# Performance work log

Measured on AMD Instinct MI355X. Metric: run time of the kernel, lower is better.

## Reference

```python
import jax, jax.numpy as jnp
import numpy as np

NUM_HEADS = 16
D_MODEL = 1024
D_K = D_MODEL // NUM_HEADS


def setup_inputs() -> dict:
    key = jax.random.key(0)
    ks = jax.random.split(key, 12)
    B, S = 2, 2048
    scale = 1.0 / np.sqrt(D_MODEL)
    inp = {
        "query": jax.random.normal(ks[0], (B, S, D_MODEL), jnp.float32),
        "key": jax.random.normal(ks[1], (B, S, D_MODEL), jnp.float32),
        "value": jax.random.normal(ks[2], (B, S, D_MODEL), jnp.float32),
        "mask": jnp.ones((B, S, S), jnp.int32),
        "Wq": jax.random.normal(ks[3], (D_MODEL, D_MODEL), jnp.float32) * scale,
        "bq": jax.random.normal(ks[4], (D_MODEL,), jnp.float32) * scale,
        "Wk": jax.random.normal(ks[5], (D_MODEL, D_MODEL), jnp.float32) * scale,
        "bk": jax.random.normal(ks[6], (D_MODEL,), jnp.float32) * scale,
        "Wv": jax.random.normal(ks[7], (D_MODEL, D_MODEL), jnp.float32) * scale,
        "bv": jax.random.normal(ks[8], (D_MODEL,), jnp.float32) * scale,
        "Wo": jax.random.normal(ks[9], (D_MODEL, D_MODEL), jnp.float32) * scale,
        "bo": jax.random.normal(ks[10], (D_MODEL,), jnp.float32) * scale,
    }
    return inp


def _split_heads(x):
    B, S, _ = x.shape
    return x.reshape(B, S, NUM_HEADS, D_K).transpose(0, 2, 1, 3)  # [B,H,S,d_k]


def reference(query, key, value, mask, Wq, bq, Wk, bk, Wv, bv, Wo, bo):
    # torch Linear: y = x @ W.T + b
    q = _split_heads(query @ Wq.T + bq)
    k = _split_heads(key @ Wk.T + bk)
    v = _split_heads(value @ Wv.T + bv)
    scores = jnp.einsum("bhqd,bhkd->bhqk", q, k) / np.sqrt(D_K)
    scores = jnp.where(mask[:, None, :, :] == 0, jnp.float32(-1e9), scores)
    p_attn = jax.nn.softmax(scores, axis=-1)
    attn = jnp.einsum("bhqk,bhkd->bhqd", p_attn, v)  # [B,H,S,d_k]
    B, _, S, _ = attn.shape
    x = attn.transpose(0, 2, 1, 3).reshape(B, S, D_MODEL)
    return x @ Wo.T + bo
```

## Files before the change

### kernel.cpp

```cpp
#include <hip/hip_runtime.h>
#include <hip/hip_bf16.h>
#include <cstdint>

#define DEVINL static __device__ __forceinline__

typedef __attribute__((ext_vector_type(4))) float floatx4;
typedef __attribute__((ext_vector_type(8))) short bf16x8;

DEVINL unsigned short f2bf(float f) {
    union { float f; uint32_t u; } v; v.f = f;
    return (unsigned short)((v.u + 0x7FFFu + ((v.u >> 16) & 1u)) >> 16);
}

DEVINL uint32_t pk2bf(float x, float y) {
    __hip_bfloat162 h = __float22bfloat162_rn(float2{x, y});
    union { __hip_bfloat162 h; uint32_t u; } v; v.h = h;
    return v.u;
}

DEVINL floatx4 mfma16(bf16x8 a, bf16x8 b, floatx4 c) {
    return __builtin_amdgcn_mfma_f32_16x16x32_bf16(a, b, c, 0, 0, 0);
}

#define GLDS16(g, l)                                                            \
    __builtin_amdgcn_global_load_lds(                                           \
        (const __attribute__((address_space(1))) void*)(g),                     \
        (__attribute__((address_space(3))) void*)(l), 16, 0, 0)

constexpr int B_ = 2, S_ = 2048, D_ = 1024, H_ = 16, DK_ = 64;
constexpr int BSROWS = B_ * S_;
constexpr int NQB = S_ / 128;
constexpr int NKT = S_ / 64;

constexpr float QSCALE = 0.18033688011112042f;

__device__ int g_flags[B_ * NQB * NKT];

__global__ __launch_bounds__(256)
void prep(const float* __restrict__ q, const float* __restrict__ k,
          const float* __restrict__ v,
          const float* __restrict__ Wq, const float* __restrict__ Wk,
          const float* __restrict__ Wv, const float* __restrict__ Wo,
          unsigned short* __restrict__ qb, unsigned short* __restrict__ kb,
          unsigned short* __restrict__ vb,
          unsigned short* __restrict__ wqb, unsigned short* __restrict__ wkb,
          unsigned short* __restrict__ wvb, unsigned short* __restrict__ wob,
          const int* __restrict__ mask)
{
    __shared__ int f;
    int bid = blockIdx.x;
    if (bid < 8192) {
        const float* src; unsigned short* dst; int rb;
        if      (bid < 2048) { src = q;  dst = qb;  rb = bid; }
        else if (bid < 4096) { src = k;  dst = kb;  rb = bid - 2048; }
        else if (bid < 6144) { src = v;  dst = vb;  rb = bid - 4096; }
        else if (bid < 6656) { src = Wq; dst = wqb; rb = bid - 6144; }
        else if (bid < 7168) { src = Wk; dst = wkb; rb = bid - 6656; }
        else if (bid < 7680) { src = Wv; dst = wvb; rb = bid - 7168; }
        else                 { src = Wo; dst = wob; rb = bid - 7680; }
        size_t e = ((size_t)rb * 256 + threadIdx.x) * 8;
        float4 v0 = *(const float4*)(src + e);
        float4 v1 = *(const float4*)(src + e + 4);
        uint4 o;
        o.x = pk2bf(v0.x, v0.y); o.y = pk2bf(v0.z, v0.w);
        o.z = pk2bf(v1.x, v1.y); o.w = pk2bf(v1.z, v1.w);
        *(uint4*)(dst + e) = o;
    } else {
        int mb = bid - 8192;
        int kt = mb & 31, qq = (mb >> 5) & 15, b = mb >> 9;
        const int* base = mask + (size_t)(b * S_ + qq * 128) * S_ + kt * 64;
        int ok = 1;
        #pragma unroll
        for (int i = 0; i < 8; ++i) {
            int u = threadIdx.x + 256 * i;
            int row = u >> 4, c = u & 15;
            int4 m = *(const int4*)(base + (size_t)row * S_ + c * 4);
            if ((m.x == 0) | (m.y == 0) | (m.z == 0) | (m.w == 0)) ok = 0;
        }
        if (threadIdx.x == 0) f = 1;
        __syncthreads();
        if (!ok) f = 0;
        __syncthreads();
        if (threadIdx.x == 0) g_flags[mb] = f;
    }
}

__global__ __launch_bounds__(256)
void gemm_qkv(const unsigned short* __restrict__ qb, const unsigned short* __restrict__ kb,
              const unsigned short* __restrict__ vb,
              const unsigned short* __restrict__ wqb, const unsigned short* __restrict__ wkb,
              const unsigned short* __restrict__ wvb,
              const float* __restrict__ bq, const float* __restrict__ bk,
              const float* __restrict__ bv,
              unsigned short* __restrict__ Qp, unsigned short* __restrict__ KpF,
              unsigned short* __restrict__ VpF)
{
    constexpr int K = D_, N = D_;
    __shared__ unsigned short As[2][128 * 64];
    __shared__ unsigned short Bs[2][128 * 64];

    const int bid = blockIdx.x;
    const int xcd = bid & 7, sl = bid >> 3;
    const int z = sl >> 5, rr = sl & 31;
    const int nb = rr >> 2, mloc = rr & 3;
    const int m0 = (mloc * 8 + xcd) * 128, n0 = nb * 128;

    const unsigned short* A = z == 0 ? qb  : z == 1 ? kb  : vb;
    const unsigned short* W = z == 0 ? wqb : z == 1 ? wkb : wvb;
    const float* bias       = z == 0 ? bq  : z == 1 ? bk  : bv;

    const int tid  = threadIdx.x;
    const int lane = tid & 63, wave = tid >> 6;
    const int lr = lane & 15, lg = lane >> 4;
    const int wm = (wave >> 1) * 64, wn = (wave & 1) * 64;

    int rowA[4], kcA[4];
    #pragma unroll
    for (int j = 0; j < 4; ++j) {
        int L = (wave * 4 + j) * 64 + lane;
        rowA[j] = L >> 3; kcA[j] = (L & 7) ^ (rowA[j] & 7);
    }

    auto dma = [&](int k0, int buf) {
        #pragma unroll
        for (int j = 0; j < 4; ++j)
            GLDS16(A + (size_t)(m0 + rowA[j]) * K + k0 + kcA[j] * 8,
                   &As[buf][(wave * 4 + j) * 512 + lane * 8]);
        #pragma unroll
        for (int j = 0; j < 4; ++j)
            GLDS16(W + (size_t)(n0 + rowA[j]) * K + k0 + kcA[j] * 8,
                   &Bs[buf][(wave * 4 + j) * 512 + lane * 8]);
    };

    floatx4 acc[4][4];
    #pragma unroll
    for (int mt = 0; mt < 4; ++mt)
        #pragma unroll
        for (int nt = 0; nt < 4; ++nt)
            acc[mt][nt] = floatx4{0.f, 0.f, 0.f, 0.f};

    dma(0, 0);
    for (int it = 0; it < K / 64; ++it) {
        __syncthreads();
        if (it + 1 < K / 64) dma((it + 1) * 64, (it + 1) & 1);
        const int buf = it & 1;

        #pragma unroll
        for (int kf = 0; kf < 2; ++kf) {
            bf16x8 af[4], bfr[4];
            #pragma unroll
            for (int mt = 0; mt < 4; ++mt) {
                int row = wm + mt * 16 + lr;
                af[mt] = *(const bf16x8*)&As[buf][row * 64 + (((kf * 4 + lg) ^ (lr & 7)) * 8)];
            }
            #pragma unroll
            for (int nt = 0; nt < 4; ++nt) {
                int row = wn + nt * 16 + lr;
                bfr[nt] = *(const bf16x8*)&Bs[buf][row * 64 + (((kf * 4 + lg) ^ (lr & 7)) * 8)];
            }
            #pragma unroll
            for (int mt = 0; mt < 4; ++mt)
                #pragma unroll
                for (int nt = 0; nt < 4; ++nt)
                    acc[mt][nt] = mfma16(af[mt], bfr[nt], acc[mt][nt]);
        }
    }

    if (z == 0) {
        #pragma unroll
        for (int nt = 0; nt < 4; ++nt) {
            int col = n0 + wn + nt * 16 + lr;
            float bv2 = bias[col];
            #pragma unroll
            for (int mt = 0; mt < 4; ++mt)
                #pragma unroll
                for (int reg = 0; reg < 4; ++reg) {
                    int row = m0 + wm + mt * 16 + lg * 4 + reg;
                    Qp[(size_t)row * N + col] = f2bf((acc[mt][nt][reg] + bv2) * QSCALE);
                }
        }
    } else if (z == 1) {
        #pragma unroll
        for (int nt = 0; nt < 4; ++nt) {
            int c = n0 + wn + nt * 16 + lr;
            int h = c >> 6, d = c & 63;
            int kfA = d >> 5, lgA = (d >> 3) & 3, j = d & 7;
            float bv2 = bias[c];
            #pragma unroll
            for (int mt = 0; mt < 4; ++mt)
                #pragma unroll
                for (int reg = 0; reg < 4; ++reg) {
                    int t = m0 + wm + mt * 16 + lg * 4 + reg;
                    int bb = t >> 11, sx = t & (S_ - 1);
                    int kt = sx >> 6, key = sx & 63;
                    int mtA = key >> 4, lrA = key & 15;
                    size_t off = (((size_t)(bb * 16 + h) * 32 + kt) * 8 + (kfA * 4 + mtA)) * 512
                               + (lrA + 16 * lgA) * 8 + j;
                    KpF[off] = f2bf(acc[mt][nt][reg] + bv2);
                }
        }
    } else {
        #pragma unroll
        for (int nt = 0; nt < 4; ++nt) {
            int c = n0 + wn + nt * 16 + lr;
            int h = c >> 6, dtA = (c >> 4) & 3;
            float bv2 = bias[c];
            #pragma unroll
            for (int mt = 0; mt < 4; ++mt) {
                int t0 = m0 + wm + mt * 16 + lg * 4;
                int bb = t0 >> 11, s0 = t0 & (S_ - 1);
                int kt = s0 >> 6, key = s0 & 63;
                int kfA = key >> 5, lgA = (key >> 3) & 3, j0 = key & 7;
                size_t off = (((size_t)(bb * 16 + h) * 32 + kt) * 8 + (dtA * 2 + kfA)) * 512
                           + (lr + 16 * lgA) * 8 + j0;
                uint2 p;
                p.x = pk2bf(acc[mt][nt][0] + bv2, acc[mt][nt][1] + bv2);
                p.y = pk2bf(acc[mt][nt][2] + bv2, acc[mt][nt][3] + bv2);
                *(uint2*)&VpF[off] = p;
            }
        }
    }
}

__global__ __launch_bounds__(256, 2)
void attn_flash(const unsigned short* __restrict__ Qp,
                const unsigned short* __restrict__ KpF,
                const unsigned short* __restrict__ VpF,
                const int* __restrict__ mask,
                unsigned short* __restrict__ Out)
{
    constexpr int LD = 72;
    __shared__ unsigned short Ps[128 * LD];

    const int tid = threadIdx.x;
    const int lane = tid & 63, wave = tid >> 6;
    const int lr = lane & 15, lg = lane >> 4;
    const int h = blockIdx.x, qb = blockIdx.y, b = blockIdx.z;
    const int q0 = qb * 128, qw = q0 + wave * 32;

    bf16x8 qf[2][2];
    #pragma unroll
    for (int qt = 0; qt < 2; ++qt)
        #pragma unroll
        for (int kf = 0; kf < 2; ++kf)
            qf[qt][kf] = *(const bf16x8*)(Qp + (size_t)(b * S_ + qw + qt * 16 + lr) * D_ +
                                          h * DK_ + kf * 32 + lg * 8);

    float l_[2] = {0.f, 0.f};
    floatx4 o_acc[2][4];
    #pragma unroll
    for (int qt = 0; qt < 2; ++qt)
        #pragma unroll
        for (int dt = 0; dt < 4; ++dt) o_acc[qt][dt] = floatx4{0.f, 0.f, 0.f, 0.f};

    const unsigned short* kbase = KpF + (size_t)(b * 16 + h) * 32 * 4096 + lane * 8;
    const unsigned short* vbase = VpF + (size_t)(b * 16 + h) * 32 * 4096 + lane * 8;
    const int fbase = (b * NQB + qb) * NKT;
    unsigned short* PsW = &Ps[(wave * 32 + lr) * LD];

    auto loadKV = [&](int kt, bf16x8 (&kfr)[8], bf16x8 (&vfr)[8]) {
        const unsigned short* kb = kbase + kt * 4096;
        const unsigned short* vb = vbase + kt * 4096;
        #pragma unroll
        for (int c = 0; c < 8; ++c) kfr[c] = *(const bf16x8*)(kb + c * 512);
        #pragma unroll
        for (int c = 0; c < 8; ++c) vfr[c] = *(const bf16x8*)(vb + c * 512);
    };

    auto process = [&](int kt, bf16x8 (&kfr)[8], bf16x8 (&vfr)[8]) {
        floatx4 sc[2][4];
        #pragma unroll
        for (int qt = 0; qt < 2; ++qt)
            #pragma unroll
            for (int mt = 0; mt < 4; ++mt) sc[qt][mt] = floatx4{0.f, 0.f, 0.f, 0.f};
        #pragma unroll
        for (int mt = 0; mt < 4; ++mt)
            #pragma unroll
            for (int kf = 0; kf < 2; ++kf)
                #pragma unroll
                for (int qt = 0; qt < 2; ++qt)
                    sc[qt][mt] = mfma16(kfr[kf * 4 + mt], qf[qt][kf], sc[qt][mt]);

        if (g_flags[fbase + kt] == 0) {
            #pragma unroll
            for (int qt = 0; qt < 2; ++qt) {
                int qq = qw + qt * 16 + lr;
                const int* mrow = mask + (size_t)(b * S_ + qq) * S_ + kt * 64;
                #pragma unroll
                for (int mt = 0; mt < 4; ++mt)
                    #pragma unroll
                    for (int reg = 0; reg < 4; ++reg)
                        if (mrow[mt * 16 + lg * 4 + reg] == 0)
                            sc[qt][mt][reg] = -1e9f;
            }
        }

        #pragma unroll
        for (int qt = 0; qt < 2; ++qt) {
            #pragma unroll
            for (int mt = 0; mt < 4; ++mt) {
                float p0 = __builtin_amdgcn_exp2f(sc[qt][mt][0]);
                float p1 = __builtin_amdgcn_exp2f(sc[qt][mt][1]);
                float p2 = __builtin_amdgcn_exp2f(sc[qt][mt][2]);
                float p3 = __builtin_amdgcn_exp2f(sc[qt][mt][3]);
                l_[qt] += (p0 + p1) + (p2 + p3);
                uint2 pk; pk.x = pk2bf(p0, p1); pk.y = pk2bf(p2, p3);
                *(uint2*)&PsW[qt * 16 * LD + mt * 16 + lg * 4] = pk;
            }
        }

        bf16x8 pb[2][2];
        #pragma unroll
        for (int qt = 0; qt < 2; ++qt)
            #pragma unroll
            for (int kf = 0; kf < 2; ++kf)
                pb[qt][kf] = *(const bf16x8*)&PsW[qt * 16 * LD + kf * 32 + lg * 8];
        #pragma unroll
        for (int dt = 0; dt < 4; ++dt)
            #pragma unroll
            for (int kf = 0; kf < 2; ++kf)
                #pragma unroll
                for (int qt = 0; qt < 2; ++qt)
                    o_acc[qt][dt] = mfma16(vfr[dt * 2 + kf], pb[qt][kf], o_acc[qt][dt]);
    };

    bf16x8 kA[8], vA[8], kB[8], vB[8];
    loadKV(0, kA, vA);
    for (int kt = 0; kt < NKT; kt += 2) {
        loadKV(kt + 1, kB, vB);
        process(kt, kA, vA);
        if (kt + 2 < NKT) loadKV(kt + 2, kA, vA);
        process(kt + 1, kB, vB);
    }

    #pragma unroll
    for (int qt = 0; qt < 2; ++qt) {
        float l = l_[qt];
        l += __shfl_xor(l, 16, 64);
        l += __shfl_xor(l, 32, 64);
        float inv = 1.f / l;
        int qq = qw + qt * 16 + lr;
        #pragma unroll
        for (int dt = 0; dt < 4; ++dt) {
            uint2 p;
            p.x = pk2bf(o_acc[qt][dt][0] * inv, o_acc[qt][dt][1] * inv);
            p.y = pk2bf(o_acc[qt][dt][2] * inv, o_acc[qt][dt][3] * inv);
            *(uint2*)&Out[(size_t)(b * S_ + qq) * D_ + h * DK_ + dt * 16 + lg * 4] = p;
        }
    }
}

__global__ __launch_bounds__(256)
void gemm_out(const unsigned short* __restrict__ Ap,
              const unsigned short* __restrict__ Wb,
              const float* __restrict__ bias, float* __restrict__ Cptr)
{
    constexpr int K = D_, N = D_;
    __shared__ unsigned short As[2][128 * 64];
    __shared__ unsigned short Wss[2][64 * 64];

    const int bid = blockIdx.x;
    const int xcd = bid & 7, sl = bid >> 3;
    const int nb = sl >> 2, mloc = sl & 3;
    const int m0 = (mloc * 8 + xcd) * 128, n0 = nb * 64;

    const int tid  = threadIdx.x;
    const int lane = tid & 63, wave = tid >> 6;
    const int lr = lane & 15, lg = lane >> 4;
    const int wm = (wave >> 1) * 64, wn = (wave & 1) * 32;

    int rowA[4], kcA[4], rowW[2], kcW[2];
    #pragma unroll
    for (int j = 0; j < 4; ++j) {
        int L = (wave * 4 + j) * 64 + lane;
        rowA[j] = L >> 3; kcA[j] = (L & 7) ^ (rowA[j] & 7);
    }
    #pragma unroll
    for (int j = 0; j < 2; ++j) {
        int L = (wave * 2 + j) * 64 + lane;
        rowW[j] = L >> 3; kcW[j] = (L & 7) ^ (rowW[j] & 7);
    }

    auto dma = [&](int k0, int buf) {
        #pragma unroll
        for (int j = 0; j < 4; ++j)
            GLDS16(Ap + (size_t)(m0 + rowA[j]) * K + k0 + kcA[j] * 8,
                   &As[buf][(wave * 4 + j) * 512 + lane * 8]);
        #pragma unroll
        for (int j = 0; j < 2; ++j)
            GLDS16(Wb + (size_t)(n0 + rowW[j]) * K + k0 + kcW[j] * 8,
                   &Wss[buf][(wave * 2 + j) * 512 + lane * 8]);
    };

    floatx4 acc[4][2];
    #pragma unroll
    for (int mt = 0; mt < 4; ++mt)
        #pragma unroll
        for (int nt = 0; nt < 2; ++nt)
            acc[mt][nt] = floatx4{0.f, 0.f, 0.f, 0.f};

    dma(0, 0);
    for (int it = 0; it < K / 64; ++it) {
        __syncthreads();
        if (it + 1 < K / 64) dma((it + 1) * 64, (it + 1) & 1);
        const int buf = it & 1;

        #pragma unroll
        for (int kf = 0; kf < 2; ++kf) {
            bf16x8 af[4], bfr[2];
            #pragma unroll
            for (int mt = 0; mt < 4; ++mt) {
                int row = wm + mt * 16 + lr;
                af[mt] = *(const bf16x8*)&As[buf][row * 64 + (((kf * 4 + lg) ^ (lr & 7)) * 8)];
            }
            #pragma unroll
            for (int nt = 0; nt < 2; ++nt) {
                int row = wn + nt * 16 + lr;
                bfr[nt] = *(const bf16x8*)&Wss[buf][row * 64 + (((kf * 4 + lg) ^ (lr & 7)) * 8)];
            }
            #pragma unroll
            for (int mt = 0; mt < 4; ++mt)
                #pragma unroll
                for (int nt = 0; nt < 2; ++nt)
                    acc[mt][nt] = mfma16(af[mt], bfr[nt], acc[mt][nt]);
        }
    }

    #pragma unroll
    for (int nt = 0; nt < 2; ++nt) {
        int col = n0 + wn + nt * 16 + lr;
        float bv2 = bias[col];
        #pragma unroll
        for (int mt = 0; mt < 4; ++mt)
            #pragma unroll
            for (int reg = 0; reg < 4; ++reg) {
                int row = m0 + wm + mt * 16 + lg * 4 + reg;
                Cptr[(size_t)row * N + col] = acc[mt][nt][reg] + bv2;
            }
    }
}

extern "C" void kernel_launch(void* const* d_in, const int* in_sizes, int n_in,
                              void* d_out, int out_size, void* d_ws, size_t ws_size,
                              hipStream_t stream)
{
    const float* query = (const float*)d_in[0];
    const float* key   = (const float*)d_in[1];
    const float* value = (const float*)d_in[2];
    const int*   mask  = (const int*)d_in[3];
    const float* Wq = (const float*)d_in[4];
    const float* bq = (const float*)d_in[5];
    const float* Wk = (const float*)d_in[6];
    const float* bk = (const float*)d_in[7];
    const float* Wv = (const float*)d_in[8];
    const float* bv = (const float*)d_in[9];
    const float* Wo = (const float*)d_in[10];
    const float* bo = (const float*)d_in[11];

    unsigned short* qb  = (unsigned short*)d_ws;
    unsigned short* kb  = qb  + (size_t)BSROWS * D_;
    unsigned short* vb  = kb  + (size_t)BSROWS * D_;
    unsigned short* wqb = vb  + (size_t)BSROWS * D_;
    unsigned short* wkb = wqb + (size_t)D_ * D_;
    unsigned short* wvb = wkb + (size_t)D_ * D_;
    unsigned short* wob = wvb + (size_t)D_ * D_;
    unsigned short* Qp  = wob + (size_t)D_ * D_;
    unsigned short* KpF = Qp  + (size_t)BSROWS * D_;
    unsigned short* VpF = KpF + (size_t)BSROWS * D_;
    unsigned short* Ap  = qb;

    dim3 blk(256);

    hipLaunchKernelGGL(prep, dim3(8192 + 1024), blk, 0, stream,
                       query, key, value, Wq, Wk, Wv, Wo,
                       qb, kb, vb, wqb, wkb, wvb, wob, mask);

    hipLaunchKernelGGL(gemm_qkv, dim3(768), blk, 0, stream,
                       qb, kb, vb, wqb, wkb, wvb, bq, bk, bv, Qp, KpF, VpF);

    dim3 gattn(H_, NQB, B_);
    hipLaunchKernelGGL(attn_flash, gattn, blk, 0, stream, Qp, KpF, VpF, mask, Ap);

    hipLaunchKernelGGL(gemm_out, dim3(512), blk, 0, stream, Ap, wob, bo, (float*)d_out);
}
```

Before: 260.8 us.

## Fuse fp32-to-bf16 conversion into GEMM loads and drop separate prep kernel

Removes the prep kernel that converted inputs and weights to bf16. The QKV and output GEMMs now load fp32 tiles into registers, convert them to bf16, and store them to LDS through a two-deep software pipeline. The mask-flag scan moves into extra blocks of the QKV GEMM launch. This saves one launch and the write-then-reread of bf16 copies, but the GEMMs read twice as many bytes per tile from global memory. Staging through registers also replaces the direct global-to-LDS loads and raises register pressure (launch_bounds 256,2).

After: 250.4 us. 4.0% less time.

```diff
diff --git a/kernel.cpp b/kernel.cpp
--- a/kernel.cpp
+++ b/kernel.cpp
@@ -36,78 +36,52 @@
 
 __device__ int g_flags[B_ * NQB * NKT];
 
-__global__ __launch_bounds__(256)
-void prep(const float* __restrict__ q, const float* __restrict__ k,
-          const float* __restrict__ v,
-          const float* __restrict__ Wq, const float* __restrict__ Wk,
-          const float* __restrict__ Wv, const float* __restrict__ Wo,
-          unsigned short* __restrict__ qb, unsigned short* __restrict__ kb,
-          unsigned short* __restrict__ vb,
-          unsigned short* __restrict__ wqb, unsigned short* __restrict__ wkb,
-          unsigned short* __restrict__ wvb, unsigned short* __restrict__ wob,
-          const int* __restrict__ mask)
-{
-    __shared__ int f;
-    int bid = blockIdx.x;
-    if (bid < 8192) {
-        const float* src; unsigned short* dst; int rb;
-        if      (bid < 2048) { src = q;  dst = qb;  rb = bid; }
-        else if (bid < 4096) { src = k;  dst = kb;  rb = bid - 2048; }
-        else if (bid < 6144) { src = v;  dst = vb;  rb = bid - 4096; }
-        else if (bid < 6656) { src = Wq; dst = wqb; rb = bid - 6144; }
-        else if (bid < 7168) { src = Wk; dst = wkb; rb = bid - 6656; }
-        else if (bid < 7680) { src = Wv; dst = wvb; rb = bid - 7168; }
-        else                 { src = Wo; dst = wob; rb = bid - 7680; }
-        size_t e = ((size_t)rb * 256 + threadIdx.x) * 8;
-        float4 v0 = *(const float4*)(src + e);
-        float4 v1 = *(const float4*)(src + e + 4);
-        uint4 o;
-        o.x = pk2bf(v0.x, v0.y); o.y = pk2bf(v0.z, v0.w);
-        o.z = pk2bf(v1.x, v1.y); o.w = pk2bf(v1.z, v1.w);
-        *(uint4*)(dst + e) = o;
-    } else {
-        int mb = bid - 8192;
-        int kt = mb & 31, qq = (mb >> 5) & 15, b = mb >> 9;
-        const int* base = mask + (size_t)(b * S_ + qq * 128) * S_ + kt * 64;
-        int ok = 1;
-        #pragma unroll
-        for (int i = 0; i < 8; ++i) {
-            int u = threadIdx.x + 256 * i;
-            int row = u >> 4, c = u & 15;
-            int4 m = *(const int4*)(base + (size_t)row * S_ + c * 4);
-            if ((m.x == 0) | (m.y == 0) | (m.z == 0) | (m.w == 0)) ok = 0;
-        }
-        if (threadIdx.x == 0) f = 1;
-        __syncthreads();
-        if (!ok) f = 0;
-        __syncthreads();
-        if (threadIdx.x == 0) g_flags[mb] = f;
-    }
-}
-
-__global__ __launch_bounds__(256)
-void gemm_qkv(const unsigned short* __restrict__ qb, const unsigned short* __restrict__ kb,
-              const unsigned short* __restrict__ vb,
-              const unsigned short* __restrict__ wqb, const unsigned short* __restrict__ wkb,
-              const unsigned short* __restrict__ wvb,
+__global__ __launch_bounds__(256, 2)
+void gemm_qkv(const float* __restrict__ q, const float* __restrict__ k,
+              const float* __restrict__ v,
+              const float* __restrict__ Wq, const float* __restrict__ Wk,
+              const float* __restrict__ Wv,
               const float* __restrict__ bq, const float* __restrict__ bk,
               const float* __restrict__ bv,
+              const int* __restrict__ mask,
               unsigned short* __restrict__ Qp, unsigned short* __restrict__ KpF,
               unsigned short* __restrict__ VpF)
 {
     constexpr int K = D_, N = D_;
     __shared__ unsigned short As[2][128 * 64];
     __shared__ unsigned short Bs[2][128 * 64];
+    __shared__ int fflag;
 
     const int bid = blockIdx.x;
+
+    if (bid >= 768) {
+        int mb = bid - 768;
+        int kt = mb & 31, qq = (mb >> 5) & 15, b = mb >> 9;
+        const int* base = mask + (size_t)(b * S_ + qq * 128) * S_ + kt * 64;
+        int ok = 1;
+        #pragma unroll
+        for (int i = 0; i < 8; ++i) {
+            int u = threadIdx.x + 256 * i;
+            int row = u >> 4, c = u & 15;
+            int4 m = *(const int4*)(base + (size_t)row * S_ + c * 4);
+            if ((m.x == 0) | (m.y == 0) | (m.z == 0) | (m.w == 0)) ok = 0;
+        }
+        if (threadIdx.x == 0) fflag = 1;
+        __syncthreads();
+        if (!ok) fflag = 0;
+        __syncthreads();
+        if (threadIdx.x == 0) g_flags[mb] = fflag;
+        return;
+    }
+
     const int xcd = bid & 7, sl = bid >> 3;
     const int z = sl >> 5, rr = sl & 31;
     const int nb = rr >> 2, mloc = rr & 3;
     const int m0 = (mloc * 8 + xcd) * 128, n0 = nb * 128;
 
-    const unsigned short* A = z == 0 ? qb  : z == 1 ? kb  : vb;
-    const unsigned short* W = z == 0 ? wqb : z == 1 ? wkb : wvb;
-    const float* bias       = z == 0 ? bq  : z == 1 ? bk  : bv;
+    const float* A    = z == 0 ? q  : z == 1 ? k  : v;
+    const float* W    = z == 0 ? Wq : z == 1 ? Wk : Wv;
+    const float* bias = z == 0 ? bq : z == 1 ? bk : bv;
 
     const int tid  = threadIdx.x;
     const int lane = tid & 63, wave = tid >> 6;
@@ -121,15 +95,30 @@
         rowA[j] = L >> 3; kcA[j] = (L & 7) ^ (rowA[j] & 7);
     }
 
-    auto dma = [&](int k0, int buf) {
-        #pragma unroll
-        for (int j = 0; j < 4; ++j)
-            GLDS16(A + (size_t)(m0 + rowA[j]) * K + k0 + kcA[j] * 8,
-                   &As[buf][(wave * 4 + j) * 512 + lane * 8]);
-        #pragma unroll
-        for (int j = 0; j < 4; ++j)
-            GLDS16(W + (size_t)(n0 + rowA[j]) * K + k0 + kcA[j] * 8,
-                   &Bs[buf][(wave * 4 + j) * 512 + lane * 8]);
+    float4 ra[4][2], rw[4][2];
+    auto loadStage = [&](int k0) {
+        #pragma unroll
+        for (int j = 0; j < 4; ++j) {
+            const float* pa = A + (size_t)(m0 + rowA[j]) * K + k0 + kcA[j] * 8;
+            ra[j][0] = *(const float4*)pa;
+            ra[j][1] = *(const float4*)(pa + 4);
+            const float* pw = W + (size_t)(n0 + rowA[j]) * K + k0 + kcA[j] * 8;
+            rw[j][0] = *(const float4*)pw;
+            rw[j][1] = *(const float4*)(pw + 4);
+        }
+    };
+    auto writeStage = [&](int buf) {
+        #pragma unroll
+        for (int j = 0; j < 4; ++j) {
+            uint4 o;
+            o.x = pk2bf(ra[j][0].x, ra[j][0].y); o.y = pk2bf(ra[j][0].z, ra[j][0].w);
+            o.z = pk2bf(ra[j][1].x, ra[j][1].y); o.w = pk2bf(ra[j][1].z, ra[j][1].w);
+            *(uint4*)&As[buf][(wave * 4 + j) * 512 + lane * 8] = o;
+            uint4 p;
+            p.x = pk2bf(rw[j][0].x, rw[j][0].y); p.y = pk2bf(rw[j][0].z, rw[j][0].w);
+            p.z = pk2bf(rw[j][1].x, rw[j][1].y); p.w = pk2bf(rw[j][1].z, rw[j][1].w);
+            *(uint4*)&Bs[buf][(wave * 4 + j) * 512 + lane * 8] = p;
+        }
     };
 
     floatx4 acc[4][4];
@@ -139,11 +128,14 @@
         for (int nt = 0; nt < 4; ++nt)
             acc[mt][nt] = floatx4{0.f, 0.f, 0.f, 0.f};
 
-    dma(0, 0);
+    loadStage(0);
+    writeStage(0);
+    loadStage(64);
+    __syncthreads();
     for (int it = 0; it < K / 64; ++it) {
-        __syncthreads();
-        if (it + 1 < K / 64) dma((it + 1) * 64, (it + 1) & 1);
         const int buf = it & 1;
+        if (it + 1 < K / 64) writeStage(buf ^ 1);
+        if (it + 2 < K / 64) loadStage((it + 2) * 64);
 
         #pragma unroll
         for (int kf = 0; kf < 2; ++kf) {
@@ -164,6 +156,7 @@
                 for (int nt = 0; nt < 4; ++nt)
                     acc[mt][nt] = mfma16(af[mt], bfr[nt], acc[mt][nt]);
         }
+        __syncthreads();
     }
 
     if (z == 0) {
@@ -352,7 +345,7 @@
 
 __global__ __launch_bounds__(256)
 void gemm_out(const unsigned short* __restrict__ Ap,
-              const unsigned short* __restrict__ Wb,
+              const float* __restrict__ Wo,
               const float* __restrict__ bias, float* __restrict__ Cptr)
 {
     constexpr int K = D_, N = D_;
@@ -381,15 +374,30 @@
         rowW[j] = L >> 3; kcW[j] = (L & 7) ^ (rowW[j] & 7);
     }
 
-    auto dma = [&](int k0, int buf) {
+    auto dmaA = [&](int k0, int buf) {
         #pragma unroll
         for (int j = 0; j < 4; ++j)
             GLDS16(Ap + (size_t)(m0 + rowA[j]) * K + k0 + kcA[j] * 8,
                    &As[buf][(wave * 4 + j) * 512 + lane * 8]);
-        #pragma unroll
-        for (int j = 0; j < 2; ++j)
-            GLDS16(Wb + (size_t)(n0 + rowW[j]) * K + k0 + kcW[j] * 8,
-                   &Wss[buf][(wave * 2 + j) * 512 + lane * 8]);
+    };
+
+    float4 rw[2][2];
+    auto loadW = [&](int k0) {
+        #pragma unroll
+        for (int j = 0; j < 2; ++j) {
+            const float* pw = Wo + (size_t)(n0 + rowW[j]) * K + k0 + kcW[j] * 8;
+            rw[j][0] = *(const float4*)pw;
+            rw[j][1] = *(const float4*)(pw + 4);
+        }
+    };
+    auto writeW = [&](int buf) {
+        #pragma unroll
+        for (int j = 0; j < 2; ++j) {
+            uint4 p;
+            p.x = pk2bf(rw[j][0].x, rw[j][0].y); p.y = pk2bf(rw[j][0].z, rw[j][0].w);
+            p.z = pk2bf(rw[j][1].x, rw[j][1].y); p.w = pk2bf(rw[j][1].z, rw[j][1].w);
+            *(uint4*)&Wss[buf][(wave * 2 + j) * 512 + lane * 8] = p;
+        }
     };
 
     floatx4 acc[4][2];
@@ -399,11 +407,13 @@
         for (int nt = 0; nt < 2; ++nt)
             acc[mt][nt] = floatx4{0.f, 0.f, 0.f, 0.f};
 
-    dma(0, 0);
+    dmaA(0, 0);
+    loadW(0); writeW(0); loadW(64);
+    __syncthreads();
     for (int it = 0; it < K / 64; ++it) {
-        __syncthreads();
-        if (it + 1 < K / 64) dma((it + 1) * 64, (it + 1) & 1);
         const int buf = it & 1;
+        if (it + 1 < K / 64) { dmaA((it + 1) * 64, buf ^ 1); writeW(buf ^ 1); }
+        if (it + 2 < K / 64) loadW((it + 2) * 64);
 
         #pragma unroll
         for (int kf = 0; kf < 2; ++kf) {
@@ -424,6 +434,7 @@
                 for (int nt = 0; nt < 2; ++nt)
                     acc[mt][nt] = mfma16(af[mt], bfr[nt], acc[mt][nt]);
         }
+        __syncthreads();
     }
 
     #pragma unroll
@@ -457,29 +468,19 @@
     const float* Wo = (const float*)d_in[10];
     const float* bo = (const float*)d_in[11];
 
-    unsigned short* qb  = (unsigned short*)d_ws;
-    unsigned short* kb  = qb  + (size_t)BSROWS * D_;
-    unsigned short* vb  = kb  + (size_t)BSROWS * D_;
-    unsigned short* wqb = vb  + (size_t)BSROWS * D_;
-    unsigned short* wkb = wqb + (size_t)D_ * D_;
-    unsigned short* wvb = wkb + (size_t)D_ * D_;
-    unsigned short* wob = wvb + (size_t)D_ * D_;
-    unsigned short* Qp  = wob + (size_t)D_ * D_;
+    unsigned short* Qp  = (unsigned short*)d_ws;
     unsigned short* KpF = Qp  + (size_t)BSROWS * D_;
     unsigned short* VpF = KpF + (size_t)BSROWS * D_;
-    unsigned short* Ap  = qb;
+    unsigned short* Ap  = VpF + (size_t)BSROWS * D_;
 
     dim3 blk(256);
 
-    hipLaunchKernelGGL(prep, dim3(8192 + 1024), blk, 0, stream,
-                       query, key, value, Wq, Wk, Wv, Wo,
-                       qb, kb, vb, wqb, wkb, wvb, wob, mask);
-
-    hipLaunchKernelGGL(gemm_qkv, dim3(768), blk, 0, stream,
-                       qb, kb, vb, wqb, wkb, wvb, bq, bk, bv, Qp, KpF, VpF);
+    hipLaunchKernelGGL(gemm_qkv, dim3(768 + 1024), blk, 0, stream,
+                       query, key, value, Wq, Wk, Wv, bq, bk, bv, mask,
+                       Qp, KpF, VpF);
 
     dim3 gattn(H_, NQB, B_);
     hipLaunchKernelGGL(attn_flash, gattn, blk, 0, stream, Qp, KpF, VpF, mask, Ap);
 
-    hipLaunchKernelGGL(gemm_out, dim3(512), blk, 0, stream, Ap, wob, bo, (float*)d_out);
-}
+    hipLaunchKernelGGL(gemm_out, dim3(512), blk, 0, stream, Ap, Wo, bo, (float*)d_out);
+}
```
